# Kernel tuning notes

Measured on AMD Instinct MI355X. Metric: run time of the kernel, lower is better.

## Reference

```python
import jax, jax.numpy as jnp
import numpy as np
from jax import lax

WINDOW_SIZE = 11
SIGMA = 1.5
CHANNELS = 3
C1 = 0.01 ** 2
C2 = 0.03 ** 2


def _create_window():
    coords = jnp.arange(WINDOW_SIZE, dtype=jnp.float32) - WINDOW_SIZE // 2
    g = jnp.exp(-coords ** 2 / (2.0 * SIGMA ** 2))
    g = g / g.sum()
    w2d = g[:, None] * g[None, :]                      # (11, 11)
    # depthwise kernel, OIHW with groups=channels -> (C, 1, k, k)
    return jnp.broadcast_to(w2d, (CHANNELS, 1, WINDOW_SIZE, WINDOW_SIZE))


def _dwconv(x, window):
    pad = WINDOW_SIZE // 2
    return lax.conv_general_dilated(
        x, window,
        window_strides=(1, 1),
        padding=[(pad, pad), (pad, pad)],
        dimension_numbers=('NCHW', 'OIHW', 'NCHW'),
        feature_group_count=CHANNELS,
    )


def setup_inputs() -> dict:
    key = jax.random.key(0)
    k1, k2 = jax.random.split(key)
    pred = jax.random.uniform(k1, (32, 3, 512, 512), dtype=jnp.float32)
    target = jax.random.uniform(k2, (32, 3, 512, 512), dtype=jnp.float32)
    return {"pred": pred, "target": target}


def reference(pred, target):
    pred = pred.astype(jnp.float32)
    target = target.astype(jnp.float32)
    window = _create_window()

    mu1 = _dwconv(pred, window)
    mu2 = _dwconv(target, window)
    mu1_sq = mu1 * mu1
    mu2_sq = mu2 * mu2
    mu1_mu2 = mu1 * mu2
    sigma1_sq = _dwconv(pred * pred, window) - mu1_sq
    sigma2_sq = _dwconv(target * target, window) - mu2_sq
    sigma12 = _dwconv(pred * target, window) - mu1_mu2

    ssim_map = ((2.0 * mu1_mu2 + C1) * (2.0 * sigma12 + C2)) / (
        (mu1_sq + mu2_sq + C1) * (sigma1_sq + sigma2_sq + C2))
    return 1.0 - ssim_map.mean()
```

## Files before the change

kernel.cpp:

```cpp
#include <hip/hip_runtime.h>
#include <hip/hip_bf16.h>
#include <math.h>

#define BLOCK 256
#define IMG 512
#define SW 88
#define NBLOCKS 3072
#define NACC 128
#define N_TOTAL 25165824.0f

typedef float f32x4 __attribute__((ext_vector_type(4)));
typedef short s16x8 __attribute__((ext_vector_type(8)));
typedef short s16x4 __attribute__((ext_vector_type(4)));

struct WB { unsigned short b[11]; float c2; float k1; float k2; };
union FR  { unsigned int u[4]; s16x8 s; };
union FR2 { unsigned int u[2]; s16x4 s; };

#if __has_builtin(__builtin_amdgcn_mfma_f32_16x16x16bf16_1k)
#define MFMA16(A,B,C) __builtin_amdgcn_mfma_f32_16x16x16bf16_1k((A),(B),(C),0,0,0)
#else
__device__ __forceinline__ f32x4 mfma16_asm(s16x4 a, s16x4 b, f32x4 c) {
    f32x4 d;
    asm("v_mfma_f32_16x16x16_bf16 %0, %1, %2, %3" : "=v"(d) : "v"(a), "v"(b), "v"(c));
    return d;
}
#define MFMA16(A,B,C) mfma16_asm((A),(B),(C))
#endif

#define WG_SYNC() do { \
    asm volatile("s_waitcnt lgkmcnt(0)" ::: "memory"); \
    __builtin_amdgcn_s_barrier(); \
    asm volatile("" ::: "memory"); \
} while (0)

__device__ __forceinline__ unsigned int pk2(float a, float b) {
    union { __hip_bfloat162 h; unsigned int u; } cv;
    cv.h = __float22bfloat162_rn(make_float2(a, b));
    return cv.u;
}

__device__ __forceinline__ void stage4(unsigned short (*sq)[16][SW],
                                       int r, int i, float4 xv, float4 yv) {
    *(uint2*)&sq[0][r][4*i] = make_uint2(pk2(xv.x,xv.y), pk2(xv.z,xv.w));
    *(uint2*)&sq[1][r][4*i] = make_uint2(pk2(yv.x,yv.y), pk2(yv.z,yv.w));
    *(uint2*)&sq[2][r][4*i] = make_uint2(
        pk2(xv.x*xv.x + yv.x*yv.x, xv.y*xv.y + yv.y*yv.y),
        pk2(xv.z*xv.z + yv.z*yv.z, xv.w*xv.w + yv.w*yv.w));
    *(uint2*)&sq[3][r][4*i] = make_uint2(pk2(xv.x*yv.x, xv.y*yv.y),
                                         pk2(xv.z*yv.z, xv.w*yv.w));
}

__device__ __forceinline__ void load_set(const float* __restrict__ P,
                                         const float* __restrict__ T,
                                         int R0, int step,
                                         int rA, int colA, bool okcA,
                                         bool hasB, int rB, int colB, bool okcB,
                                         float4& xA, float4& yA, float4& xB, float4& yB) {
    const int gr = R0 - 5 + 16 * step + rA;
    if (okcA && gr >= 0 && gr < IMG) {
        xA = *(const float4*)(P + ((size_t)gr << 9) + colA);
        yA = *(const float4*)(T + ((size_t)gr << 9) + colA);
    } else { xA = make_float4(0,0,0,0); yA = make_float4(0,0,0,0); }
    const int grB = R0 - 5 + 16 * step + rB;
    if (hasB && okcB && grB >= 0 && grB < IMG) {
        xB = *(const float4*)(P + ((size_t)grB << 9) + colB);
        yB = *(const float4*)(T + ((size_t)grB << 9) + colB);
    } else { xB = make_float4(0,0,0,0); yB = make_float4(0,0,0,0); }
}

#define H_PHASE(CUR, QB)                                                     \
  do {                                                                       \
    FR a0_, a1_, a2_, a3_;                                                   \
    a0_.s = *(const s16x8*)&s_q[QB][0][l15][hoff];                           \
    a1_.s = *(const s16x8*)&s_q[QB][1][l15][hoff];                           \
    a2_.s = *(const s16x8*)&s_q[QB][2][l15][hoff];                           \
    a3_.s = *(const s16x8*)&s_q[QB][3][l15][hoff];                           \
    f32x4 d0_ = __builtin_amdgcn_mfma_f32_16x16x32_bf16(a0_.s, bw.s, z,0,0,0);\
    f32x4 d1_ = __builtin_amdgcn_mfma_f32_16x16x32_bf16(a1_.s, bw.s, z,0,0,0);\
    f32x4 d2_ = __builtin_amdgcn_mfma_f32_16x16x32_bf16(a2_.s, bw.s, z,0,0,0);\
    f32x4 d3_ = __builtin_amdgcn_mfma_f32_16x16x32_bf16(a3_.s, bw.s, z,0,0,0);\
    CUR[0].u[0]=pk2(d0_[0],d0_[1]); CUR[0].u[1]=pk2(d0_[2],d0_[3]);          \
    CUR[1].u[0]=pk2(d1_[0],d1_[1]); CUR[1].u[1]=pk2(d1_[2],d1_[3]);          \
    CUR[2].u[0]=pk2(d2_[0],d2_[1]); CUR[2].u[1]=pk2(d2_[2],d2_[3]);          \
    CUR[3].u[0]=pk2(d3_[0],d3_[1]); CUR[3].u[1]=pk2(d3_[2],d3_[3]);          \
  } while (0)

#define V_PHASE(CUR, PRV)                                                    \
  do {                                                                       \
    f32x4 c0_ = MFMA16(awhi.s, CUR[0].s, z);                                 \
    f32x4 c1_ = MFMA16(awhi.s, CUR[1].s, z);                                 \
    f32x4 c2_ = MFMA16(awhi.s, CUR[2].s, z);                                 \
    f32x4 c3_ = MFMA16(awhi.s, CUR[3].s, z);                                 \
    c0_ = MFMA16(awlo.s, PRV[0].s, c0_);                                     \
    c1_ = MFMA16(awlo.s, PRV[1].s, c1_);                                     \
    c2_ = MFMA16(awlo.s, PRV[2].s, c2_);                                     \
    c3_ = MFMA16(awlo.s, PRV[3].s, c3_);                                     \
    _Pragma("unroll")                                                        \
    for (int i = 0; i < 4; ++i) {                                            \
        const float u1   = c0_[i];                                           \
        const float u2   = c1_[i];                                           \
        const float m11  = u1 * u1;                                          \
        const float m22  = u2 * u2;                                          \
        const float m12  = u1 * u2;                                          \
        const float esum = c2_[i] * c2;                         \
        const float e12  = c3_[i] * c2;                                      \
        const float A_ = fmaf(2.f, m12, K1);                                 \
        const float B_ = fmaf(2.f, e12 - m12, K2);                           \
        const float C_ = m11 + m22 + K1;                                     \
        const float D_ = esum - (m11 + m22) + K2;                            \
        lsum = fmaf(A_ * B_, __builtin_amdgcn_rcpf(C_ * D_), lsum);          \
    }                                                                        \
  } while (0)

#define STEP(S, CUR, PRV, QB)                                                \
  do {                                                                       \
    if ((S) < 8)                                                             \
        load_set(P, T, R0, (S) + 1, rA, colA, okcA, hasB, rB, colB, okcB,    \
                 nxA, nyA, nxB, nyB);                                        \
    H_PHASE(CUR, QB);                                                        \
    if ((S) >= 1) V_PHASE(CUR, PRV);                                         \
    if ((S) < 8) {                                                           \
        stage4(s_q[1 - (QB)], rA, iA, nxA, nyA);                             \
        if (hasB) stage4(s_q[1 - (QB)], rB, iB, nxB, nyB);                   \
        WG_SYNC();                                                           \
    }                                                                        \
  } while (0)

__global__ __launch_bounds__(BLOCK, 4)
void ssim_tiled(const float* __restrict__ pred,
                const float* __restrict__ targ,
                float* __restrict__ accum, WB wb) {
    __shared__ unsigned short s_q[2][4][16][SW];

    const int tid = threadIdx.x;
    const int bx    = blockIdx.x;
    const int plane = bx >> 5;
    const int rem   = bx & 31;
    const int tx    = rem >> 2;
    const int ry    = rem & 3;
    const int C0    = tx * 64;
    const int R0    = ry * 128;

    const float* P = pred + (size_t)plane * (IMG * IMG);
    const float* T = targ + (size_t)plane * (IMG * IMG);

    const int w    = tid >> 6;
    const int lane = tid & 63;
    const int l15  = lane & 15;
    const int quad = lane >> 4;
    const int hoff = 16 * w + 8 * quad;

    const int slotA = w * 80 + lane;
    const int rA = slotA / 20, iA = slotA % 20;
    const int colA = C0 - 8 + 4 * iA;
    const bool okcA = (colA >= 0) && (colA + 4 <= IMG);
    const bool hasB = (lane < 16);
    const int slotB = w * 80 + 64 + l15;
    const int rB = slotB / 20, iB = slotB % 20;
    const int colB = C0 - 8 + 4 * iB;
    const bool okcB = (colB >= 0) && (colB + 4 <= IMG);

    const float c2 = wb.c2, K1 = wb.k1, K2 = wb.k2;
    const f32x4 z = {0.f, 0.f, 0.f, 0.f};
    float lsum = 0.f;

    float4 nxA, nyA, nxB, nyB;
    load_set(P, T, R0, 0, rA, colA, okcA, hasB, rB, colB, okcB, nxA, nyA, nxB, nyB);

    FR bw; FR2 awlo, awhi;
    {
        const int ti = lane & 31;
        int tv = 0;
#pragma unroll
        for (int k = 0; k < 11; ++k) tv = (ti == k) ? (int)wb.b[k] : tv;
        const int tnext = __shfl(tv, (lane + 1) & 63);
        const int pairT = (tv & 0xffff) | (tnext << 16);
        const int base_b = 8 * quad - l15 - 3;
        const int baseL  = 4 * quad - l15;
        const int baseH  = 4 * quad - l15 + 16;
#pragma unroll
        for (int t = 0; t < 4; ++t)
            bw.u[t] = (unsigned int)__shfl(pairT, (base_b + 2 * t) & 63);
#pragma unroll
        for (int t = 0; t < 2; ++t) {
            awlo.u[t] = (unsigned int)__shfl(pairT, (baseL + 2 * t) & 63);
            awhi.u[t] = (unsigned int)__shfl(pairT, (baseH + 2 * t) & 63);
        }
    }

    stage4(s_q[0], rA, iA, nxA, nyA);
    if (hasB) stage4(s_q[0], rB, iB, nxB, nyB);
    WG_SYNC();

    FR2 vbE[4], vbO[4];

    STEP(0, vbE, vbO, 0);
    STEP(1, vbO, vbE, 1);
    STEP(2, vbE, vbO, 0);
    STEP(3, vbO, vbE, 1);
    STEP(4, vbE, vbO, 0);
    STEP(5, vbO, vbE, 1);
    STEP(6, vbE, vbO, 0);
    STEP(7, vbO, vbE, 1);
    STEP(8, vbE, vbO, 0);

#pragma unroll
    for (int off = 32; off > 0; off >>= 1) lsum += __shfl_down(lsum, off, 64);
    if (lane == 0) atomicAdd(&accum[(bx * 4 + w) & (NACC - 1)], lsum);
}

__global__ void ssim_finalize(const float* __restrict__ accum, float* __restrict__ out) {
    const int l = threadIdx.x;
    float v = accum[l] + accum[l + 64];
#pragma unroll
    for (int off = 32; off > 0; off >>= 1) v += __shfl_down(v, off, 64);
    if (l == 0) out[0] = 1.0f - v * (1.0f / N_TOTAL);
}

extern "C" void kernel_launch(void* const* d_in, const int* in_sizes, int n_in,
                              void* d_out, int out_size, void* d_ws, size_t ws_size,
                              hipStream_t stream) {
    const float* pred = (const float*)d_in[0];
    const float* targ = (const float*)d_in[1];
    float* out = (float*)d_out;
    float* ws  = (float*)d_ws;

    WB wb;
    {
        double gg[11], sum = 0.0;
        for (int k = 0; k < 11; ++k) {
            const double d = (double)(k - 5);
            gg[k] = exp(-d * d / 4.5);
            sum += gg[k];
        }
        double sbf = 0.0;
        for (int k = 0; k < 11; ++k) {
            union { float f; unsigned int u; } cv;
            cv.f = (float)(gg[k] / sum);
            const unsigned int r = (cv.u + 0x7fffu + ((cv.u >> 16) & 1u)) >> 16;
            wb.b[k] = (unsigned short)r;
            union { float f; unsigned int u; } bk;
            bk.u = r << 16;
            sbf += (double)bk.f;
        }
        const double s2 = sbf * sbf;
        wb.c2 = (float)s2;
        wb.k1 = (float)(0.0001 * s2 * s2);
        wb.k2 = (float)(0.0009 * s2 * s2);
    }

    hipMemsetAsync(ws, 0, NACC * sizeof(float), stream);
    ssim_tiled<<<NBLOCKS, BLOCK, 0, stream>>>(pred, targ, ws, wb);
    ssim_finalize<<<1, 64, 0, stream>>>(ws, out);
}
```

Measured before the change: 265.2 us.

## Give each wave a private LDS tile and drop workgroup barriers

Each wave now loads and stages its own 16x32 column slab (including halo) into a per-wave LDS buffer instead of sharing a block-wide tile. This removes the workgroup barriers between steps. Global loads are prefetched two steps ahead using register double-buffering. In exchange, halo columns are loaded redundantly by neighbouring waves, register pressure rises, and correctness now depends on in-wave LDS ordering without explicit waitcnt/barrier.

```diff
diff --git a/kernel.cpp b/kernel.cpp
--- a/kernel.cpp
+++ b/kernel.cpp
@@ -4,7 +4,6 @@
 
 #define BLOCK 256
 #define IMG 512
-#define SW 88
 #define NBLOCKS 3072
 #define NACC 128
 #define N_TOTAL 25165824.0f
@@ -28,54 +27,49 @@
 #define MFMA16(A,B,C) mfma16_asm((A),(B),(C))
 #endif
 
-#define WG_SYNC() do { \
-    asm volatile("s_waitcnt lgkmcnt(0)" ::: "memory"); \
-    __builtin_amdgcn_s_barrier(); \
-    asm volatile("" ::: "memory"); \
-} while (0)
-
 __device__ __forceinline__ unsigned int pk2(float a, float b) {
     union { __hip_bfloat162 h; unsigned int u; } cv;
     cv.h = __float22bfloat162_rn(make_float2(a, b));
     return cv.u;
 }
 
-__device__ __forceinline__ void stage4(unsigned short (*sq)[16][SW],
-                                       int r, int i, float4 xv, float4 yv) {
-    *(uint2*)&sq[0][r][4*i] = make_uint2(pk2(xv.x,xv.y), pk2(xv.z,xv.w));
-    *(uint2*)&sq[1][r][4*i] = make_uint2(pk2(yv.x,yv.y), pk2(yv.z,yv.w));
-    *(uint2*)&sq[2][r][4*i] = make_uint2(
-        pk2(xv.x*xv.x + yv.x*yv.x, xv.y*xv.y + yv.y*yv.y),
-        pk2(xv.z*xv.z + yv.z*yv.z, xv.w*xv.w + yv.w*yv.w));
-    *(uint2*)&sq[3][r][4*i] = make_uint2(pk2(xv.x*yv.x, xv.y*yv.y),
-                                         pk2(xv.z*yv.z, xv.w*yv.w));
-}
-
-__device__ __forceinline__ void load_set(const float* __restrict__ P,
-                                         const float* __restrict__ T,
-                                         int R0, int step,
-                                         int rA, int colA, bool okcA,
-                                         bool hasB, int rB, int colB, bool okcB,
-                                         float4& xA, float4& yA, float4& xB, float4& yB) {
-    const int gr = R0 - 5 + 16 * step + rA;
-    if (okcA && gr >= 0 && gr < IMG) {
-        xA = *(const float4*)(P + ((size_t)gr << 9) + colA);
-        yA = *(const float4*)(T + ((size_t)gr << 9) + colA);
-    } else { xA = make_float4(0,0,0,0); yA = make_float4(0,0,0,0); }
-    const int grB = R0 - 5 + 16 * step + rB;
-    if (hasB && okcB && grB >= 0 && grB < IMG) {
-        xB = *(const float4*)(P + ((size_t)grB << 9) + colB);
-        yB = *(const float4*)(T + ((size_t)grB << 9) + colB);
-    } else { xB = make_float4(0,0,0,0); yB = make_float4(0,0,0,0); }
-}
-
-#define H_PHASE(CUR, QB)                                                     \
-  do {                                                                       \
+
+#define LOADW(S, X0, X1, Y0, Y1) do {                                        \
+    const int gr_ = R0 - 5 + 16 * (S) + sr;                                  \
+    const bool okr_ = (gr_ >= 0) && (gr_ < IMG);                             \
+    const float* bp_ = P + ((size_t)gr_ << 9) + col;                         \
+    const float* bt_ = T + ((size_t)gr_ << 9) + col;                         \
+    X0 = (okr_ && ok0) ? *(const float4*)bp_       : make_float4(0,0,0,0);   \
+    X1 = (okr_ && ok1) ? *(const float4*)(bp_ + 4) : make_float4(0,0,0,0);   \
+    Y0 = (okr_ && ok0) ? *(const float4*)bt_       : make_float4(0,0,0,0);   \
+    Y1 = (okr_ && ok1) ? *(const float4*)(bt_ + 4) : make_float4(0,0,0,0);   \
+} while (0)
+
+#define STAGEW(X0, X1, Y0, Y1) do {                                          \
+    uint4 mx_ = make_uint4(pk2(X0.x,X0.y), pk2(X0.z,X0.w),                   \
+                           pk2(X1.x,X1.y), pk2(X1.z,X1.w));                  \
+    uint4 my_ = make_uint4(pk2(Y0.x,Y0.y), pk2(Y0.z,Y0.w),                   \
+                           pk2(Y1.x,Y1.y), pk2(Y1.z,Y1.w));                  \
+    uint4 ms_ = make_uint4(                                                  \
+        pk2(X0.x*X0.x+Y0.x*Y0.x, X0.y*X0.y+Y0.y*Y0.y),                       \
+        pk2(X0.z*X0.z+Y0.z*Y0.z, X0.w*X0.w+Y0.w*Y0.w),                       \
+        pk2(X1.x*X1.x+Y1.x*Y1.x, X1.y*X1.y+Y1.y*Y1.y),                       \
+        pk2(X1.z*X1.z+Y1.z*Y1.z, X1.w*X1.w+Y1.w*Y1.w));                      \
+    uint4 mp_ = make_uint4(                                                  \
+        pk2(X0.x*Y0.x, X0.y*Y0.y), pk2(X0.z*Y0.z, X0.w*Y0.w),               \
+        pk2(X1.x*Y1.x, X1.y*Y1.y), pk2(X1.z*Y1.z, X1.w*Y1.w));               \
+    *(uint4*)&s_p[w][0][sr][cb] = mx_;                                       \
+    *(uint4*)&s_p[w][1][sr][cb] = my_;                                       \
+    *(uint4*)&s_p[w][2][sr][cb] = ms_;                                       \
+    *(uint4*)&s_p[w][3][sr][cb] = mp_;                                       \
+} while (0)
+
+#define H_PHASE(CUR) do {                                                    \
     FR a0_, a1_, a2_, a3_;                                                   \
-    a0_.s = *(const s16x8*)&s_q[QB][0][l15][hoff];                           \
-    a1_.s = *(const s16x8*)&s_q[QB][1][l15][hoff];                           \
-    a2_.s = *(const s16x8*)&s_q[QB][2][l15][hoff];                           \
-    a3_.s = *(const s16x8*)&s_q[QB][3][l15][hoff];                           \
+    a0_.s = *(const s16x8*)&s_p[w][0][l15][8 * quad];                        \
+    a1_.s = *(const s16x8*)&s_p[w][1][l15][8 * quad];                        \
+    a2_.s = *(const s16x8*)&s_p[w][2][l15][8 * quad];                        \
+    a3_.s = *(const s16x8*)&s_p[w][3][l15][8 * quad];                        \
     f32x4 d0_ = __builtin_amdgcn_mfma_f32_16x16x32_bf16(a0_.s, bw.s, z,0,0,0);\
     f32x4 d1_ = __builtin_amdgcn_mfma_f32_16x16x32_bf16(a1_.s, bw.s, z,0,0,0);\
     f32x4 d2_ = __builtin_amdgcn_mfma_f32_16x16x32_bf16(a2_.s, bw.s, z,0,0,0);\
@@ -84,10 +78,9 @@
     CUR[1].u[0]=pk2(d1_[0],d1_[1]); CUR[1].u[1]=pk2(d1_[2],d1_[3]);          \
     CUR[2].u[0]=pk2(d2_[0],d2_[1]); CUR[2].u[1]=pk2(d2_[2],d2_[3]);          \
     CUR[3].u[0]=pk2(d3_[0],d3_[1]); CUR[3].u[1]=pk2(d3_[2],d3_[3]);          \
-  } while (0)
-
-#define V_PHASE(CUR, PRV)                                                    \
-  do {                                                                       \
+} while (0)
+
+#define V_PHASE(CUR, PRV) do {                                               \
     f32x4 c0_ = MFMA16(awhi.s, CUR[0].s, z);                                 \
     f32x4 c1_ = MFMA16(awhi.s, CUR[1].s, z);                                 \
     f32x4 c2_ = MFMA16(awhi.s, CUR[2].s, z);                                 \
@@ -111,27 +104,20 @@
         const float D_ = esum - (m11 + m22) + K2;                            \
         lsum = fmaf(A_ * B_, __builtin_amdgcn_rcpf(C_ * D_), lsum);          \
     }                                                                        \
-  } while (0)
-
-#define STEP(S, CUR, PRV, QB)                                                \
-  do {                                                                       \
-    if ((S) < 8)                                                             \
-        load_set(P, T, R0, (S) + 1, rA, colA, okcA, hasB, rB, colB, okcB,    \
-                 nxA, nyA, nxB, nyB);                                        \
-    H_PHASE(CUR, QB);                                                        \
+} while (0)
+
+#define STEP(S, CUR, PRV, LX0,LX1,LY0,LY1, TX0,TX1,TY0,TY1) do {             \
+    if ((S) < 7) LOADW((S) + 2, LX0, LX1, LY0, LY1);                         \
+    H_PHASE(CUR);                                                            \
     if ((S) >= 1) V_PHASE(CUR, PRV);                                         \
-    if ((S) < 8) {                                                           \
-        stage4(s_q[1 - (QB)], rA, iA, nxA, nyA);                             \
-        if (hasB) stage4(s_q[1 - (QB)], rB, iB, nxB, nyB);                   \
-        WG_SYNC();                                                           \
-    }                                                                        \
-  } while (0)
+    if ((S) < 8) STAGEW(TX0, TX1, TY0, TY1);                                 \
+} while (0)
 
 __global__ __launch_bounds__(BLOCK, 4)
 void ssim_tiled(const float* __restrict__ pred,
                 const float* __restrict__ targ,
                 float* __restrict__ accum, WB wb) {
-    __shared__ unsigned short s_q[2][4][16][SW];
+    __shared__ __align__(16) unsigned short s_p[4][4][16][32];
 
     const int tid = threadIdx.x;
     const int bx    = blockIdx.x;
@@ -149,24 +135,21 @@
     const int lane = tid & 63;
     const int l15  = lane & 15;
     const int quad = lane >> 4;
-    const int hoff = 16 * w + 8 * quad;
-
-    const int slotA = w * 80 + lane;
-    const int rA = slotA / 20, iA = slotA % 20;
-    const int colA = C0 - 8 + 4 * iA;
-    const bool okcA = (colA >= 0) && (colA + 4 <= IMG);
-    const bool hasB = (lane < 16);
-    const int slotB = w * 80 + 64 + l15;
-    const int rB = slotB / 20, iB = slotB % 20;
-    const int colB = C0 - 8 + 4 * iB;
-    const bool okcB = (colB >= 0) && (colB + 4 <= IMG);
+    const int sr   = lane >> 2;
+    const int cb   = (lane & 3) * 8;
+
+    const int col = C0 + 16 * w - 8 + cb;
+    const bool ok0 = (col >= 0) && (col + 4 <= IMG);
+    const bool ok1 = (col + 4 >= 0) && (col + 8 <= IMG);
 
     const float c2 = wb.c2, K1 = wb.k1, K2 = wb.k2;
     const f32x4 z = {0.f, 0.f, 0.f, 0.f};
     float lsum = 0.f;
 
-    float4 nxA, nyA, nxB, nyB;
-    load_set(P, T, R0, 0, rA, colA, okcA, hasB, rB, colB, okcB, nxA, nyA, nxB, nyB);
+    float4 pX0, pX1, pY0, pY1;
+    float4 qX0, qX1, qY0, qY1;
+    LOADW(0, pX0, pX1, pY0, pY1);
+    LOADW(1, qX0, qX1, qY0, qY1);
 
     FR bw; FR2 awlo, awhi;
     {
@@ -189,21 +172,19 @@
         }
     }
 
-    stage4(s_q[0], rA, iA, nxA, nyA);
-    if (hasB) stage4(s_q[0], rB, iB, nxB, nyB);
-    WG_SYNC();
+    STAGEW(pX0, pX1, pY0, pY1);
 
     FR2 vbE[4], vbO[4];
 
-    STEP(0, vbE, vbO, 0);
-    STEP(1, vbO, vbE, 1);
-    STEP(2, vbE, vbO, 0);
-    STEP(3, vbO, vbE, 1);
-    STEP(4, vbE, vbO, 0);
-    STEP(5, vbO, vbE, 1);
-    STEP(6, vbE, vbO, 0);
-    STEP(7, vbO, vbE, 1);
-    STEP(8, vbE, vbO, 0);
+    STEP(0, vbE, vbO, pX0,pX1,pY0,pY1, qX0,qX1,qY0,qY1);
+    STEP(1, vbO, vbE, qX0,qX1,qY0,qY1, pX0,pX1,pY0,pY1);
+    STEP(2, vbE, vbO, pX0,pX1,pY0,pY1, qX0,qX1,qY0,qY1);
+    STEP(3, vbO, vbE, qX0,qX1,qY0,qY1, pX0,pX1,pY0,pY1);
+    STEP(4, vbE, vbO, pX0,pX1,pY0,pY1, qX0,qX1,qY0,qY1);
+    STEP(5, vbO, vbE, qX0,qX1,qY0,qY1, pX0,pX1,pY0,pY1);
+    STEP(6, vbE, vbO, pX0,pX1,pY0,pY1, qX0,qX1,qY0,qY1);
+    STEP(7, vbO, vbE, qX0,qX1,qY0,qY1, pX0,pX1,pY0,pY1);
+    STEP(8, vbE, vbO, pX0,pX1,pY0,pY1, qX0,qX1,qY0,qY1);
 
 #pragma unroll
     for (int off = 32; off > 0; off >>= 1) lsum += __shfl_down(lsum, off, 64);
```

After: 288.4 us. 1.09x slower.
